# Kernel optimization log

Hardware: AMD Instinct MI355X
Metric: run time of the kernel (lower is better)

The kernel has to match this reference:

```python
import jax, jax.numpy as jnp
import numpy as np

D = 2          # spatial / tensor dimension (k=1 vector images)
GROUPS = 8     # channel groups
EPS = 1e-05


def setup_inputs() -> dict:
    key = jax.random.key(0)
    kx, kb = jax.random.split(key)
    x = jax.random.normal(kx, (16, 64, 128, 128, D), dtype=jnp.float32)
    scale = jnp.ones((64, 1, 1, 1), dtype=jnp.float32)
    bias = jax.random.normal(kb, (64, 1, 1, 1), dtype=jnp.float32)
    return {"x": x, "scale": scale, "bias": bias}


def reference(x, scale, bias):
    # x: (batch, channels, H, W, D) vector (k=1) image block
    batch, in_c = x.shape[:2]
    spatial = x.shape[2:2 + D]
    cpg = in_c // GROUPS  # channels per group

    # mean vector over spatial dims only, per (batch, channel): (b, c, 1, 1, D)
    mean_vec = jnp.mean(x, axis=tuple(range(2, 2 + D)), keepdims=True)

    # group channels: (b, g, cpg, H, W, D)
    xg = x.reshape((batch, GROUPS, cpg) + spatial + (D,))
    # mean over (cpg, H, W) per group, keeping the D tensor axis
    mean = jnp.mean(xg, axis=tuple(range(2, 3 + D)), keepdims=True)
    centered = xg - mean

    # flatten to (b, g, n, D) with n = cpg*H*W
    Xf = centered.reshape(batch, GROUPS, -1, D)
    n = Xf.shape[2]
    # per-group DxD covariance
    cov = jnp.einsum('bgnj,bgnk->bgjk', Xf, Xf) / n

    # whitening via symmetric eigendecomposition (equivariant, unlike cholesky)
    eigvals, eigvecs = jnp.linalg.eigh(cov, symmetrize_input=False)
    s = jnp.sqrt(1.0 / (eigvals + EPS))  # (b, g, D)
    # W = V diag(s) V^T  (same math as the original chained einsum)
    Wm = jnp.einsum('bgij,bgj,bgkj->bgik', eigvecs, s, eigvecs)
    whitened = jnp.einsum('bgik,bgnk->bgni', Wm, Xf).reshape(x.shape)

    # equivariant affine: scale * whitened + bias * (spatial mean vector)
    return whitened * scale + bias * mean_vec
```

## Files before the change

kernel.cpp:

```cpp
#include <hip/hip_runtime.h>

#define BATCH 16
#define CH 64
#define NGROUPS 8
#define CPG 8
#define HWPIX (128*128)
#define DD 2
#define EPSV 1e-5f
#define SPLIT 4
#define SPLITN 4
#define TPB 256

typedef float fx4 __attribute__((ext_vector_type(4)));


__global__ __launch_bounds__(TPB) void gn_stats(const float* __restrict__ x,
                                                float* __restrict__ partials) {
    const int blk = blockIdx.x;
    const int sp  = blk % SPLIT;
    const int bc  = blk / SPLIT;
    const int F4_PER_CH = HWPIX * DD / 4;
    const int CHUNK     = F4_PER_CH / SPLIT;
    const fx4* base = (const fx4*)x + (size_t)bc * F4_PER_CH + (size_t)sp * CHUNK;
    const int tid = threadIdx.x;

    float s0 = 0.f, s1 = 0.f, sxx = 0.f, sxy = 0.f, syy = 0.f;
    const int PER_THREAD = CHUNK / TPB;
#pragma unroll
    for (int i = 0; i < PER_THREAD; ++i) {
        fx4 v = base[tid + i * TPB];
        s0 += v.x + v.z;
        s1 += v.y + v.w;
        sxx = fmaf(v.x, v.x, fmaf(v.z, v.z, sxx));
        sxy = fmaf(v.x, v.y, fmaf(v.z, v.w, sxy));
        syy = fmaf(v.y, v.y, fmaf(v.w, v.w, syy));
    }
#pragma unroll
    for (int off = 32; off > 0; off >>= 1) {
        s0  += __shfl_down(s0, off);
        s1  += __shfl_down(s1, off);
        sxx += __shfl_down(sxx, off);
        sxy += __shfl_down(sxy, off);
        syy += __shfl_down(syy, off);
    }
    __shared__ float red[4][5];
    const int wave = tid >> 6, lane = tid & 63;
    if (lane == 0) {
        red[wave][0] = s0; red[wave][1] = s1; red[wave][2] = sxx;
        red[wave][3] = sxy; red[wave][4] = syy;
    }
    __syncthreads();
    if (tid == 0) {
        float r0 = 0.f, r1 = 0.f, r2 = 0.f, r3 = 0.f, r4 = 0.f;
#pragma unroll
        for (int w = 0; w < 4; ++w) {
            r0 += red[w][0]; r1 += red[w][1]; r2 += red[w][2];
            r3 += red[w][3]; r4 += red[w][4];
        }
        float* p = partials + (size_t)(bc * SPLIT + sp) * 5;
        p[0] = r0; p[1] = r1; p[2] = r2; p[3] = r3; p[4] = r4;
    }
}

__global__ __launch_bounds__(TPB) void gn_norm(const float* __restrict__ x,
                                               const float* __restrict__ partials,
                                               const float* __restrict__ scale,
                                               const float* __restrict__ bias,
                                               float* __restrict__ out) {
    const int blk = blockIdx.x;
    const int sp  = blk % SPLITN;
    const int bc  = blk / SPLITN;
    const int c   = bc % CH;
    const int b   = bc / CH;
    const int g   = c / CPG;
    const int cig = c % CPG;

    const int F4_PER_CH = HWPIX * DD / 4;
    const int CHUNK     = F4_PER_CH / SPLITN;
    const fx4* src = (const fx4*)x + (size_t)bc * F4_PER_CH + (size_t)sp * CHUNK;
    fx4*       dst = (fx4*)out     + (size_t)bc * F4_PER_CH + (size_t)sp * CHUNK;
    const int tid = threadIdx.x;
    const int PER_THREAD = CHUNK / TPB;

    fx4 v[PER_THREAD];
#pragma unroll
    for (int i = 0; i < PER_THREAD; ++i) v[i] = src[tid + i * TPB];

    __shared__ float coef[5];
    if (tid < 32) {
        const float* p = partials +
            ((size_t)(b * CH + g * CPG + (tid >> 2)) * SPLIT + (tid & 3)) * 5;
        float p0 = p[0], p1 = p[1], p2 = p[2], p3 = p[3], p4 = p[4];
        const bool mine = (tid >> 2) == cig;
        float q0 = mine ? p0 : 0.f, q1 = mine ? p1 : 0.f;
#pragma unroll
        for (int off = 16; off > 0; off >>= 1) {
            p0 += __shfl_xor(p0, off, 32);
            p1 += __shfl_xor(p1, off, 32);
            p2 += __shfl_xor(p2, off, 32);
            p3 += __shfl_xor(p3, off, 32);
            p4 += __shfl_xor(p4, off, 32);
            q0 += __shfl_xor(q0, off, 32);
            q1 += __shfl_xor(q1, off, 32);
        }
        if (tid == 0) {
            const float n  = (float)(CPG * HWPIX);
            const float m0 = p0 / n, m1 = p1 / n;
            const float a  = p2 / n - m0 * m0 + EPSV;
            const float bq = p3 / n - m0 * m1;
            const float cc = p4 / n - m1 * m1 + EPSV;
            const float sdet = sqrtf(a * cc - bq * bq);
            const float t    = sqrtf(a + cc + 2.0f * sdet);
            const float inv  = 1.0f / (sdet * t);
            const float w00 = (cc + sdet) * inv;
            const float w01 = -bq * inv;
            const float w11 = (a + sdet) * inv;
            const float sc = scale[c], bi = bias[c];
            const float mv0 = q0 / (float)HWPIX, mv1 = q1 / (float)HWPIX;
            const float a00 = sc * w00, a01 = sc * w01, a11 = sc * w11;
            coef[0] = a00;
            coef[1] = a01;
            coef[2] = a11;
            coef[3] = fmaf(bi, mv0, -(a00 * m0 + a01 * m1));
            coef[4] = fmaf(bi, mv1, -(a01 * m0 + a11 * m1));
        }
    }
    __syncthreads();
    const float a00 = coef[0], a01 = coef[1], a11 = coef[2];
    const float add0 = coef[3], add1 = coef[4];

#pragma unroll
    for (int i = 0; i < PER_THREAD; ++i) {
        fx4 o;
        o.x = fmaf(a00, v[i].x, fmaf(a01, v[i].y, add0));
        o.y = fmaf(a01, v[i].x, fmaf(a11, v[i].y, add1));
        o.z = fmaf(a00, v[i].z, fmaf(a01, v[i].w, add0));
        o.w = fmaf(a01, v[i].z, fmaf(a11, v[i].w, add1));
        __builtin_nontemporal_store(o, &dst[tid + i * TPB]);
    }
}

extern "C" void kernel_launch(void* const* d_in, const int* in_sizes, int n_in,
                              void* d_out, int out_size, void* d_ws, size_t ws_size,
                              hipStream_t stream) {
    const float* x     = (const float*)d_in[0];
    const float* scale = (const float*)d_in[1];
    const float* bias  = (const float*)d_in[2];
    float* out = (float*)d_out;

    float* partials = (float*)d_ws;

    gn_stats<<<BATCH * CH * SPLIT, TPB, 0, stream>>>(x, partials);
    gn_norm<<<BATCH * CH * SPLITN, TPB, 0, stream>>>(x, partials, scale, bias, out);
}
```

Measured before the change: 64.39 us.

## Fuse stats and normalize into one cooperative kernel caching input on-chip

Replaces the two-kernel stats/normalize sequence with a single cooperative-launch kernel in which each block handles two channels. Most of each channel's data is kept in registers and LDS across a grid-wide sync, so the normalize pass mostly avoids re-reading x from memory. The cost is a grid sync, heavy register and LDS use (two blocks per CU), and host-side occupancy and attribute queries on every launch. The old two-kernel path remains as a fallback when cooperative launch is unavailable or too few blocks fit.

```diff
diff --git a/kernel.cpp b/kernel.cpp
--- a/kernel.cpp
+++ b/kernel.cpp
@@ -1,46 +1,231 @@
 #include <hip/hip_runtime.h>
+#include <hip/hip_cooperative_groups.h>
+
+namespace cg = cooperative_groups;
 
 #define BATCH 16
 #define CH 64
 #define NGROUPS 8
 #define CPG 8
 #define HWPIX (128*128)
-#define DD 2
 #define EPSV 1e-5f
+#define TPB 256
+#define F4_PER_CH (HWPIX*2/4)
+#define ITERS (F4_PER_CH/TPB)
+#define NBLK2 (BATCH*CH/2)
+#define REGI 20
+#define LDSI 8
 #define SPLIT 4
-#define SPLITN 4
-#define TPB 256
 
 typedef float fx4 __attribute__((ext_vector_type(4)));
 
+__device__ __forceinline__ void acc5(float& s0, float& s1, float& sxx,
+                                     float& sxy, float& syy, fx4 t) {
+    s0 += t.x + t.z;
+    s1 += t.y + t.w;
+    sxx = fmaf(t.x, t.x, fmaf(t.z, t.z, sxx));
+    sxy = fmaf(t.x, t.y, fmaf(t.z, t.w, sxy));
+    syy = fmaf(t.y, t.y, fmaf(t.w, t.w, syy));
+}
+
+__device__ __forceinline__ fx4 affine2(fx4 t, float a00, float a01, float a11,
+                                       float d0, float d1) {
+    fx4 o;
+    o.x = fmaf(a00, t.x, fmaf(a01, t.y, d0));
+    o.y = fmaf(a01, t.x, fmaf(a11, t.y, d1));
+    o.z = fmaf(a00, t.z, fmaf(a01, t.w, d0));
+    o.w = fmaf(a01, t.z, fmaf(a11, t.w, d1));
+    return o;
+}
+
+__device__ __forceinline__ void solve_w(float p0, float p1, float p2, float p3,
+                                        float p4, float n, float& m0, float& m1,
+                                        float& w00, float& w01, float& w11) {
+    m0 = p0 / n; m1 = p1 / n;
+    const float a  = p2 / n - m0 * m0 + EPSV;
+    const float bq = p3 / n - m0 * m1;
+    const float cc = p4 / n - m1 * m1 + EPSV;
+    const float sdet = sqrtf(a * cc - bq * bq);
+    const float t    = sqrtf(a + cc + 2.0f * sdet);
+    const float inv  = 1.0f / (sdet * t);
+    w00 = (cc + sdet) * inv;
+    w01 = -bq * inv;
+    w11 = (a + sdet) * inv;
+}
+
+__global__ __launch_bounds__(TPB, 2) void gn_fused2(const float* __restrict__ x,
+                                                    const float* __restrict__ scale,
+                                                    const float* __restrict__ bias,
+                                                    float* __restrict__ partials,
+                                                    float* __restrict__ out) {
+    const int blk = blockIdx.x;
+    const int chA = 2 * blk;
+    const int cA  = chA % CH;
+    const int b   = chA / CH;
+    const int g   = cA / CPG;
+    const int tid = threadIdx.x;
+
+    const fx4* srcA = (const fx4*)x + (size_t)chA * F4_PER_CH;
+    const fx4* srcB = srcA + F4_PER_CH;
+
+    __shared__ fx4 lcache[2 * LDSI * TPB];
+    __shared__ float red[4][10];
+    __shared__ float own[4];
+    __shared__ float coef[10];
+
+    float A0 = 0.f, A1 = 0.f, Axx = 0.f, Axy = 0.f, Ayy = 0.f;
+    float B0 = 0.f, B1 = 0.f, Bxx = 0.f, Bxy = 0.f, Byy = 0.f;
+    fx4 va[REGI], vb[REGI];
+
+#pragma unroll
+    for (int i = 0; i < REGI; ++i) {
+        fx4 t = __builtin_nontemporal_load(&srcA[i * TPB + tid]);
+        va[i] = t; acc5(A0, A1, Axx, Axy, Ayy, t);
+    }
+#pragma unroll
+    for (int i = 0; i < LDSI; ++i) {
+        fx4 t = __builtin_nontemporal_load(&srcA[(REGI + i) * TPB + tid]);
+        lcache[i * TPB + tid] = t; acc5(A0, A1, Axx, Axy, Ayy, t);
+    }
+#pragma unroll
+    for (int i = REGI + LDSI; i < ITERS; ++i) {
+        fx4 t = srcA[i * TPB + tid];
+        acc5(A0, A1, Axx, Axy, Ayy, t);
+    }
+#pragma unroll
+    for (int i = 0; i < REGI; ++i) {
+        fx4 t = __builtin_nontemporal_load(&srcB[i * TPB + tid]);
+        vb[i] = t; acc5(B0, B1, Bxx, Bxy, Byy, t);
+    }
+#pragma unroll
+    for (int i = 0; i < LDSI; ++i) {
+        fx4 t = __builtin_nontemporal_load(&srcB[(REGI + i) * TPB + tid]);
+        lcache[(LDSI + i) * TPB + tid] = t; acc5(B0, B1, Bxx, Bxy, Byy, t);
+    }
+#pragma unroll
+    for (int i = REGI + LDSI; i < ITERS; ++i) {
+        fx4 t = srcB[i * TPB + tid];
+        acc5(B0, B1, Bxx, Bxy, Byy, t);
+    }
+
+#pragma unroll
+    for (int off = 32; off > 0; off >>= 1) {
+        A0 += __shfl_down(A0, off);  A1 += __shfl_down(A1, off);
+        Axx += __shfl_down(Axx, off); Axy += __shfl_down(Axy, off);
+        Ayy += __shfl_down(Ayy, off);
+        B0 += __shfl_down(B0, off);  B1 += __shfl_down(B1, off);
+        Bxx += __shfl_down(Bxx, off); Bxy += __shfl_down(Bxy, off);
+        Byy += __shfl_down(Byy, off);
+    }
+    if ((tid & 63) == 0) {
+        const int w = tid >> 6;
+        red[w][0] = A0; red[w][1] = A1; red[w][2] = Axx; red[w][3] = Axy; red[w][4] = Ayy;
+        red[w][5] = B0; red[w][6] = B1; red[w][7] = Bxx; red[w][8] = Bxy; red[w][9] = Byy;
+    }
+    __syncthreads();
+    if (tid == 0) {
+        float r[10];
+#pragma unroll
+        for (int k = 0; k < 10; ++k)
+            r[k] = red[0][k] + red[1][k] + red[2][k] + red[3][k];
+        float* pA = partials + (size_t)chA * 5;
+        pA[0] = r[0]; pA[1] = r[1]; pA[2] = r[2]; pA[3] = r[3]; pA[4] = r[4];
+        float* pB = partials + (size_t)(chA + 1) * 5;
+        pB[0] = r[5]; pB[1] = r[6]; pB[2] = r[7]; pB[3] = r[8]; pB[4] = r[9];
+        own[0] = r[0]; own[1] = r[1]; own[2] = r[5]; own[3] = r[6];
+    }
+
+    cg::this_grid().sync();
+
+    if (tid < 8) {
+        const float* p = partials + (size_t)(b * CH + g * CPG + tid) * 5;
+        float p0 = p[0], p1 = p[1], p2 = p[2], p3 = p[3], p4 = p[4];
+#pragma unroll
+        for (int off = 4; off > 0; off >>= 1) {
+            p0 += __shfl_xor(p0, off, 8);
+            p1 += __shfl_xor(p1, off, 8);
+            p2 += __shfl_xor(p2, off, 8);
+            p3 += __shfl_xor(p3, off, 8);
+            p4 += __shfl_xor(p4, off, 8);
+        }
+        if (tid == 0) {
+            float m0, m1, w00, w01, w11;
+            solve_w(p0, p1, p2, p3, p4, (float)(CPG * HWPIX), m0, m1, w00, w01, w11);
+            const float scA = scale[cA], biA = bias[cA];
+            const float scB = scale[cA + 1], biB = bias[cA + 1];
+            const float aA00 = scA * w00, aA01 = scA * w01, aA11 = scA * w11;
+            const float aB00 = scB * w00, aB01 = scB * w01, aB11 = scB * w11;
+            coef[0] = aA00; coef[1] = aA01; coef[2] = aA11;
+            coef[3] = fmaf(biA, own[0] / (float)HWPIX, -(aA00 * m0 + aA01 * m1));
+            coef[4] = fmaf(biA, own[1] / (float)HWPIX, -(aA01 * m0 + aA11 * m1));
+            coef[5] = aB00; coef[6] = aB01; coef[7] = aB11;
+            coef[8] = fmaf(biB, own[2] / (float)HWPIX, -(aB00 * m0 + aB01 * m1));
+            coef[9] = fmaf(biB, own[3] / (float)HWPIX, -(aB01 * m0 + aB11 * m1));
+        }
+    }
+    __syncthreads();
+
+    {
+        const float a00 = coef[0], a01 = coef[1], a11 = coef[2];
+        const float d0 = coef[3], d1 = coef[4];
+        fx4* dst = (fx4*)out + (size_t)chA * F4_PER_CH;
+#pragma unroll
+        for (int i = 0; i < REGI; ++i)
+            __builtin_nontemporal_store(affine2(va[i], a00, a01, a11, d0, d1),
+                                        &dst[i * TPB + tid]);
+#pragma unroll
+        for (int i = 0; i < LDSI; ++i) {
+            fx4 t = lcache[i * TPB + tid];
+            __builtin_nontemporal_store(affine2(t, a00, a01, a11, d0, d1),
+                                        &dst[(REGI + i) * TPB + tid]);
+        }
+#pragma unroll
+        for (int i = REGI + LDSI; i < ITERS; ++i) {
+            fx4 t = srcA[i * TPB + tid];
+            __builtin_nontemporal_store(affine2(t, a00, a01, a11, d0, d1),
+                                        &dst[i * TPB + tid]);
+        }
+    }
+    {
+        const float a00 = coef[5], a01 = coef[6], a11 = coef[7];
+        const float d0 = coef[8], d1 = coef[9];
+        fx4* dst = (fx4*)out + (size_t)(chA + 1) * F4_PER_CH;
+#pragma unroll
+        for (int i = 0; i < REGI; ++i)
+            __builtin_nontemporal_store(affine2(vb[i], a00, a01, a11, d0, d1),
+                                        &dst[i * TPB + tid]);
+#pragma unroll
+        for (int i = 0; i < LDSI; ++i) {
+            fx4 t = lcache[(LDSI + i) * TPB + tid];
+            __builtin_nontemporal_store(affine2(t, a00, a01, a11, d0, d1),
+                                        &dst[(REGI + i) * TPB + tid]);
+        }
+#pragma unroll
+        for (int i = REGI + LDSI; i < ITERS; ++i) {
+            fx4 t = srcB[i * TPB + tid];
+            __builtin_nontemporal_store(affine2(t, a00, a01, a11, d0, d1),
+                                        &dst[i * TPB + tid]);
+        }
+    }
+}
 
 __global__ __launch_bounds__(TPB) void gn_stats(const float* __restrict__ x,
                                                 float* __restrict__ partials) {
     const int blk = blockIdx.x;
     const int sp  = blk % SPLIT;
     const int bc  = blk / SPLIT;
-    const int F4_PER_CH = HWPIX * DD / 4;
-    const int CHUNK     = F4_PER_CH / SPLIT;
+    const int CHUNK = F4_PER_CH / SPLIT;
     const fx4* base = (const fx4*)x + (size_t)bc * F4_PER_CH + (size_t)sp * CHUNK;
     const int tid = threadIdx.x;
 
     float s0 = 0.f, s1 = 0.f, sxx = 0.f, sxy = 0.f, syy = 0.f;
-    const int PER_THREAD = CHUNK / TPB;
-#pragma unroll
-    for (int i = 0; i < PER_THREAD; ++i) {
-        fx4 v = base[tid + i * TPB];
-        s0 += v.x + v.z;
-        s1 += v.y + v.w;
-        sxx = fmaf(v.x, v.x, fmaf(v.z, v.z, sxx));
-        sxy = fmaf(v.x, v.y, fmaf(v.z, v.w, sxy));
-        syy = fmaf(v.y, v.y, fmaf(v.w, v.w, syy));
-    }
+#pragma unroll
+    for (int i = 0; i < CHUNK / TPB; ++i)
+        acc5(s0, s1, sxx, sxy, syy, base[tid + i * TPB]);
 #pragma unroll
     for (int off = 32; off > 0; off >>= 1) {
-        s0  += __shfl_down(s0, off);
-        s1  += __shfl_down(s1, off);
-        sxx += __shfl_down(sxx, off);
-        sxy += __shfl_down(sxy, off);
+        s0 += __shfl_down(s0, off);  s1 += __shfl_down(s1, off);
+        sxx += __shfl_down(sxx, off); sxy += __shfl_down(sxy, off);
         syy += __shfl_down(syy, off);
     }
     __shared__ float red[4][5];
@@ -68,15 +253,14 @@
                                                const float* __restrict__ bias,
                                                float* __restrict__ out) {
     const int blk = blockIdx.x;
-    const int sp  = blk % SPLITN;
-    const int bc  = blk / SPLITN;
+    const int sp  = blk % SPLIT;
+    const int bc  = blk / SPLIT;
     const int c   = bc % CH;
     const int b   = bc / CH;
     const int g   = c / CPG;
     const int cig = c % CPG;
 
-    const int F4_PER_CH = HWPIX * DD / 4;
-    const int CHUNK     = F4_PER_CH / SPLITN;
+    const int CHUNK = F4_PER_CH / SPLIT;
     const fx4* src = (const fx4*)x + (size_t)bc * F4_PER_CH + (size_t)sp * CHUNK;
     fx4*       dst = (fx4*)out     + (size_t)bc * F4_PER_CH + (size_t)sp * CHUNK;
     const int tid = threadIdx.x;
@@ -95,49 +279,28 @@
         float q0 = mine ? p0 : 0.f, q1 = mine ? p1 : 0.f;
 #pragma unroll
         for (int off = 16; off > 0; off >>= 1) {
-            p0 += __shfl_xor(p0, off, 32);
-            p1 += __shfl_xor(p1, off, 32);
-            p2 += __shfl_xor(p2, off, 32);
-            p3 += __shfl_xor(p3, off, 32);
+            p0 += __shfl_xor(p0, off, 32); p1 += __shfl_xor(p1, off, 32);
+            p2 += __shfl_xor(p2, off, 32); p3 += __shfl_xor(p3, off, 32);
             p4 += __shfl_xor(p4, off, 32);
-            q0 += __shfl_xor(q0, off, 32);
-            q1 += __shfl_xor(q1, off, 32);
+            q0 += __shfl_xor(q0, off, 32); q1 += __shfl_xor(q1, off, 32);
         }
         if (tid == 0) {
-            const float n  = (float)(CPG * HWPIX);
-            const float m0 = p0 / n, m1 = p1 / n;
-            const float a  = p2 / n - m0 * m0 + EPSV;
-            const float bq = p3 / n - m0 * m1;
-            const float cc = p4 / n - m1 * m1 + EPSV;
-            const float sdet = sqrtf(a * cc - bq * bq);
-            const float t    = sqrtf(a + cc + 2.0f * sdet);
-            const float inv  = 1.0f / (sdet * t);
-            const float w00 = (cc + sdet) * inv;
-            const float w01 = -bq * inv;
-            const float w11 = (a + sdet) * inv;
+            float m0, m1, w00, w01, w11;
+            solve_w(p0, p1, p2, p3, p4, (float)(CPG * HWPIX), m0, m1, w00, w01, w11);
             const float sc = scale[c], bi = bias[c];
-            const float mv0 = q0 / (float)HWPIX, mv1 = q1 / (float)HWPIX;
             const float a00 = sc * w00, a01 = sc * w01, a11 = sc * w11;
-            coef[0] = a00;
-            coef[1] = a01;
-            coef[2] = a11;
-            coef[3] = fmaf(bi, mv0, -(a00 * m0 + a01 * m1));
-            coef[4] = fmaf(bi, mv1, -(a01 * m0 + a11 * m1));
+            coef[0] = a00; coef[1] = a01; coef[2] = a11;
+            coef[3] = fmaf(bi, q0 / (float)HWPIX, -(a00 * m0 + a01 * m1));
+            coef[4] = fmaf(bi, q1 / (float)HWPIX, -(a01 * m0 + a11 * m1));
         }
     }
     __syncthreads();
     const float a00 = coef[0], a01 = coef[1], a11 = coef[2];
-    const float add0 = coef[3], add1 = coef[4];
-
-#pragma unroll
-    for (int i = 0; i < PER_THREAD; ++i) {
-        fx4 o;
-        o.x = fmaf(a00, v[i].x, fmaf(a01, v[i].y, add0));
-        o.y = fmaf(a01, v[i].x, fmaf(a11, v[i].y, add1));
-        o.z = fmaf(a00, v[i].z, fmaf(a01, v[i].w, add0));
-        o.w = fmaf(a01, v[i].z, fmaf(a11, v[i].w, add1));
-        __builtin_nontemporal_store(o, &dst[tid + i * TPB]);
-    }
+    const float d0 = coef[3], d1 = coef[4];
+#pragma unroll
+    for (int i = 0; i < PER_THREAD; ++i)
+        __builtin_nontemporal_store(affine2(v[i], a00, a01, a11, d0, d1),
+                                    &dst[tid + i * TPB]);
 }
 
 extern "C" void kernel_launch(void* const* d_in, const int* in_sizes, int n_in,
@@ -146,10 +309,27 @@
     const float* x     = (const float*)d_in[0];
     const float* scale = (const float*)d_in[1];
     const float* bias  = (const float*)d_in[2];
-    float* out = (float*)d_out;
-
+    float* out      = (float*)d_out;
     float* partials = (float*)d_ws;
 
-    gn_stats<<<BATCH * CH * SPLIT, TPB, 0, stream>>>(x, partials);
-    gn_norm<<<BATCH * CH * SPLITN, TPB, 0, stream>>>(x, partials, scale, bias, out);
-}
+    bool coop_ok = false;
+    int dev = 0;
+    if (hipGetDevice(&dev) == hipSuccess) {
+        int has_coop = 0, ncu = 0, nblk_per_cu = 0;
+        hipDeviceGetAttribute(&has_coop, hipDeviceAttributeCooperativeLaunch, dev);
+        hipDeviceGetAttribute(&ncu, hipDeviceAttributeMultiprocessorCount, dev);
+        hipOccupancyMaxActiveBlocksPerMultiprocessor(&nblk_per_cu, gn_fused2, TPB, 0);
+        if (has_coop && (long)nblk_per_cu * ncu >= NBLK2) {
+            void* args[] = {(void*)&x, (void*)&scale, (void*)&bias,
+                            (void*)&partials, (void*)&out};
+            hipError_t e = hipLaunchCooperativeKernel((const void*)gn_fused2,
+                                                      dim3(NBLK2), dim3(TPB),
+                                                      args, 0, stream);
+            coop_ok = (e == hipSuccess);
+        }
+    }
+    if (!coop_ok) {
+        gn_stats<<<BATCH * CH * SPLIT, TPB, 0, stream>>>(x, partials);
+        gn_norm<<<BATCH * CH * SPLIT, TPB, 0, stream>>>(x, partials, scale, bias, out);
+    }
+}
```

New measurement: 64.15 us. About the same (-0.4%).
